# Performance work log

Hardware: AMD Instinct MI355X
Metric: run time of the kernel (lower is better)

## Reference

```python
import jax, jax.numpy as jnp
import numpy as np

B, T, C = 4, 2048, 1024
NUM_EXPERTS = 8
TOP_K = 2
D_EXPERT = 4 * C * TOP_K // NUM_EXPERTS  # 1024


def setup_inputs() -> dict:
    key = jax.random.key(0)
    k0, k1, k2, k3 = jax.random.split(key, 4)
    x = jax.random.normal(k0, (B, T, C), dtype=jnp.float32)
    # nn.Linear(n_embd, num_experts, bias=False).weight has shape [E, C]
    router_w = jax.random.normal(k1, (NUM_EXPERTS, C), dtype=jnp.float32) * 0.02
    # w1_all = stack of c_fc.weight.T  -> [E, C, D]
    w1_all = jax.random.normal(k2, (NUM_EXPERTS, C, D_EXPERT), dtype=jnp.float32) * 0.02
    # w2_all = stack of c_proj.weight.T -> [E, D, C]
    w2_all = jax.random.normal(k3, (NUM_EXPERTS, D_EXPERT, C), dtype=jnp.float32) * 0.02
    return {"x": x, "router_w": router_w, "w1_all": w1_all, "w2_all": w2_all}


def reference(x, router_w, w1_all, w2_all):
    b, t, c = x.shape
    x_flat = x.reshape(-1, c)                      # [N, C]
    router_logits = x_flat @ router_w.T            # [N, E]
    top_k_logits, top_k_idx = jax.lax.top_k(router_logits, TOP_K)  # [N, K]
    router_probs = jax.nn.softmax(top_k_logits, axis=-1)           # [N, K]

    # Same math as the original per-token weight gather, but computed as
    # dense all-expert GEMMs followed by an output gather (avoids the
    # [N, K, C, D] materialized weight copies while producing identical values).
    hidden = jnp.einsum('nc,ecd->ned', x_flat, w1_all)   # [N, E, D]
    hidden = jnp.square(jax.nn.relu(hidden))             # relu^2
    out_all = jnp.einsum('ned,edc->nec', hidden, w2_all) # [N, E, C]

    sel = jnp.take_along_axis(out_all, top_k_idx[:, :, None], axis=1)  # [N, K, C]
    out = jnp.sum(sel * router_probs[:, :, None], axis=1)             # [N, C]
    return out.reshape(b, t, c)
```

## Files before the change

### kernel.cpp

```cpp
#include <hip/hip_runtime.h>
#include <cstdint>
#include <cstddef>

typedef unsigned short ushort_t;
typedef unsigned short ushort8 __attribute__((ext_vector_type(8)));
typedef __bf16 bf16x8 __attribute__((ext_vector_type(8)));
typedef float floatx4 __attribute__((ext_vector_type(4)));

#define N_TOK 8192
#define CDIM 1024
#define NEXP 8

__device__ __forceinline__ float bf2f(ushort_t h) {
  union { unsigned int u; float f; } v; v.u = ((unsigned int)h) << 16; return v.f;
}
__device__ __forceinline__ ushort_t f2bf(float f) {
  union { float f; unsigned int u; } v; v.f = f;
  unsigned int r = v.u + 0x7fffu + ((v.u >> 16) & 1u);
  return (ushort_t)(r >> 16);
}

__device__ __forceinline__ void async_copy16(const ushort_t* g, ushort_t* l) {
  __builtin_amdgcn_global_load_lds(
      (const __attribute__((address_space(1))) unsigned int*)g,
      (__attribute__((address_space(3))) unsigned int*)l, 16, 0, 0);
}

__global__ void detect_init_kernel(const ushort_t* __restrict__ x,
                                   int* __restrict__ flag,
                                   int* __restrict__ cnt) {
  int tid = threadIdx.x;
  ushort_t u = x[tid];
  int ex = (u >> 7) & 0xFF;
  int crazy = (ex >= 0xC0 || ex <= 0x30) ? 1 : 0;
  int total = __syncthreads_count(crazy);
  if (tid == 0) flag[0] = (total >= 16) ? 1 : 0;
  if (tid < NEXP) cnt[tid] = 0;
}

__global__ void router_compute(const void* __restrict__ xv,
                               const void* __restrict__ rwv,
                               const int* __restrict__ flag,
                               int* __restrict__ tok_e,
                               float* __restrict__ prob,
                               ushort_t* __restrict__ xbf) {
  int isf32 = flag[0];
  int wid = threadIdx.x >> 6;
  int lane = threadIdx.x & 63;
  int t = blockIdx.x * 4 + wid;

  float acc[NEXP];
#pragma unroll
  for (int e = 0; e < NEXP; e++) acc[e] = 0.f;

  if (isf32) {
    const float* xr = (const float*)xv + (size_t)t * CDIM;
    const float* rw = (const float*)rwv;
#pragma unroll
    for (int half = 0; half < 2; half++) {
      int base = (lane + half * 64) * 8;
      floatx4 x0 = *(const floatx4*)(xr + base);
      floatx4 x1 = *(const floatx4*)(xr + base + 4);
      ushort8 o;
#pragma unroll
      for (int i = 0; i < 4; i++) { o[i] = f2bf(x0[i]); o[4 + i] = f2bf(x1[i]); }
      *(ushort8*)(xbf + (size_t)t * CDIM + base) = o;
#pragma unroll
      for (int e = 0; e < NEXP; e++) {
        floatx4 w0 = *(const floatx4*)(rw + e * CDIM + base);
        floatx4 w1 = *(const floatx4*)(rw + e * CDIM + base + 4);
        acc[e] += x0[0]*w0[0] + x0[1]*w0[1] + x0[2]*w0[2] + x0[3]*w0[3]
                + x1[0]*w1[0] + x1[1]*w1[1] + x1[2]*w1[2] + x1[3]*w1[3];
      }
    }
  } else {
    const ushort_t* xr = (const ushort_t*)xv + (size_t)t * CDIM;
    const ushort_t* rw = (const ushort_t*)rwv;
#pragma unroll
    for (int half = 0; half < 2; half++) {
      int base = (lane + half * 64) * 8;
      ushort8 xu = *(const ushort8*)(xr + base);
      *(ushort8*)(xbf + (size_t)t * CDIM + base) = xu;
#pragma unroll
      for (int e = 0; e < NEXP; e++) {
        ushort8 wu = *(const ushort8*)(rw + e * CDIM + base);
#pragma unroll
        for (int i = 0; i < 8; i++) acc[e] += bf2f(xu[i]) * bf2f(wu[i]);
      }
    }
  }

#pragma unroll
  for (int e = 0; e < NEXP; e++) {
#pragma unroll
    for (int off = 32; off > 0; off >>= 1) acc[e] += __shfl_xor(acc[e], off);
  }

  if (lane == 0) {
    int e0 = 0; float l0 = acc[0];
#pragma unroll
    for (int e = 1; e < NEXP; e++) if (acc[e] > l0) { l0 = acc[e]; e0 = e; }
    int e1 = (e0 == 0) ? 1 : 0; float l1 = acc[e1];
#pragma unroll
    for (int e = 0; e < NEXP; e++) {
      if (e != e0 && acc[e] > l1) { l1 = acc[e]; e1 = e; }
    }
    float p0 = 1.f / (1.f + __expf(l1 - l0));
    tok_e[t] = e0 | (e1 << 8);
    prob[t * 2] = p0;
    prob[t * 2 + 1] = 1.f - p0;
  }
}

__global__ void scatter_kernel(const int* __restrict__ tok_e,
                               int* __restrict__ cnt,
                               int* __restrict__ slots) {
  __shared__ int lcnt[NEXP];
  __shared__ int gbase[NEXP];
  int tid = threadIdx.x;
  if (tid < NEXP) lcnt[tid] = 0;
  __syncthreads();
  int t = blockIdx.x * 1024 + tid;
  int ee = tok_e[t];
  int e0 = ee & 0xFF, e1 = (ee >> 8) & 0xFF;
  int lofs0 = atomicAdd(&lcnt[e0], 1);
  int lofs1 = atomicAdd(&lcnt[e1], 1);
  __syncthreads();
  if (tid < NEXP) gbase[tid] = atomicAdd(&cnt[tid], lcnt[tid]);
  __syncthreads();
  slots[e0 * N_TOK + gbase[e0] + lofs0] = t * 2;
  slots[e1 * N_TOK + gbase[e1] + lofs1] = t * 2 + 1;
}

__global__ void transpose_kernel(const void* __restrict__ w1v,
                                 const void* __restrict__ w2v,
                                 const int* __restrict__ flag,
                                 ushort_t* __restrict__ w1T,
                                 ushort_t* __restrict__ w2T) {
  int isf32 = flag[0];
  int z = blockIdx.z;
  size_t moff = (size_t)(z & 7) << 20;
  const void* srcv = (z < 8) ? w1v : w2v;
  ushort_t* dst = ((z < 8) ? w1T : w2T) + moff;

  __shared__ __align__(16) ushort_t tile[64][72];
  int t = threadIdx.x;
  int R0 = blockIdx.y * 64, C0 = blockIdx.x * 64;
  int r = t >> 2, cb = (t & 3) * 16;
  if (isf32) {
    const float* sp = (const float*)srcv + moff + (size_t)(R0 + r) * 1024 + C0 + cb;
    ushort8 o0, o1;
#pragma unroll
    for (int q = 0; q < 2; q++) {
      floatx4 f = *(const floatx4*)(sp + q * 4);
#pragma unroll
      for (int i = 0; i < 4; i++) o0[q * 4 + i] = f2bf(f[i]);
    }
#pragma unroll
    for (int q = 0; q < 2; q++) {
      floatx4 f = *(const floatx4*)(sp + 8 + q * 4);
#pragma unroll
      for (int i = 0; i < 4; i++) o1[q * 4 + i] = f2bf(f[i]);
    }
    *(ushort8*)&tile[r][cb] = o0;
    *(ushort8*)&tile[r][cb + 8] = o1;
  } else {
    const ushort_t* sp = (const ushort_t*)srcv + moff + (size_t)(R0 + r) * 1024 + C0 + cb;
    *(ushort8*)&tile[r][cb] = *(const ushort8*)sp;
    *(ushort8*)&tile[r][cb + 8] = *(const ushort8*)(sp + 8);
  }
  __syncthreads();
  int d = t >> 2, rb = (t & 3) * 16;
  ushort8 o0, o1;
#pragma unroll
  for (int j = 0; j < 8; j++) { o0[j] = tile[rb + j][d]; o1[j] = tile[rb + 8 + j][d]; }
  ushort_t* dp = dst + (size_t)(C0 + d) * 1024 + R0 + rb;
  *(ushort8*)dp = o0;
  *(ushort8*)(dp + 8) = o1;
}

template <int MODE>
__global__ __launch_bounds__(512, 4) void moe_gemm(const ushort_t* __restrict__ A,
                                                   const ushort_t* __restrict__ BT,
                                                   ushort_t* __restrict__ Out,
                                                   const int* __restrict__ cnt,
                                                   const int* __restrict__ slots,
                                                   const float* __restrict__ prob) {
  int bid = blockIdx.x;
  int e = bid & 7;
  int nt = (bid >> 3) & 7;
  int mt = bid >> 6;
  int M = cnt[e];
  M = (M > N_TOK) ? N_TOK : M;
  int m0 = mt * 256;
  if (m0 >= M) return;
  int n0 = nt * 128;

  __shared__ __align__(16) ushort_t As[2][256 * 32];
  __shared__ __align__(16) ushort_t Bs[2][128 * 32];
  __shared__ int srow[256];

  int tid = threadIdx.x;
  if (tid < 256) {
    int gm = m0 + tid;
    int gi = (gm < M) ? gm : (M - 1);
    srow[tid] = slots[e * N_TOK + gi] & (2 * N_TOK - 1);
  }
  __syncthreads();

  int wid = tid >> 6;
  int lane = tid & 63;
  int lrow = lane >> 2;
  int gchunk = (lane & 3) ^ (lrow & 3);

  const ushort_t* aptr[2];
  const ushort_t* bptr0;
#pragma unroll
  for (int j = 0; j < 2; j++) {
    int rr = j * 128 + wid * 16 + lrow;
    int s = srow[rr];
    int aidx = (MODE == 0) ? (s >> 1) : s;
    aptr[j] = A + (size_t)aidx * CDIM + gchunk * 8;
  }
  {
    int rr = wid * 16 + lrow;
    bptr0 = BT + ((size_t)e << 20) + (size_t)(n0 + rr) * 1024 + gchunk * 8;
  }

  int wm = (wid >> 1) * 64;
  int wn = (wid & 1) * 64;
  int qd = lane >> 4;
  int ln = lane & 15;
  int l3 = ln & 3;
  int pc = (qd ^ l3) * 8;

  floatx4 zero = {0.f, 0.f, 0.f, 0.f};
  floatx4 acc[4][4];
#pragma unroll
  for (int i = 0; i < 4; i++)
#pragma unroll
    for (int j = 0; j < 4; j++) acc[i][j] = zero;

#define STAGE(buf, kofs)                                                     \
  do {                                                                       \
    async_copy16(aptr[0] + (kofs), &As[buf][wid * 512]);                     \
    async_copy16(aptr[1] + (kofs), &As[buf][4096 + wid * 512]);              \
    async_copy16(bptr0 + (kofs), &Bs[buf][wid * 512]);                       \
  } while (0)

#define COMPUTE(cb)                                                          \
  do {                                                                       \
    bf16x8 afr[4], bfr[4];                                                   \
    _Pragma("unroll")                                                        \
    for (int i = 0; i < 4; i++) {                                            \
      afr[i] = *(const bf16x8*)&As[cb][(wm + i * 16 + ln) * 32 + pc];        \
      bfr[i] = *(const bf16x8*)&Bs[cb][(wn + i * 16 + ln) * 32 + pc];        \
    }                                                                        \
    __builtin_amdgcn_s_setprio(1);                                           \
    _Pragma("unroll")                                                        \
    for (int i = 0; i < 4; i++)                                              \
      _Pragma("unroll")                                                      \
      for (int j = 0; j < 4; j++)                                            \
        acc[i][j] = __builtin_amdgcn_mfma_f32_16x16x32_bf16(afr[i], bfr[j],  \
                                                            acc[i][j], 0, 0, 0); \
    __builtin_amdgcn_s_setprio(0);                                           \
  } while (0)

  STAGE(0, 0);
  int cur = 0;
  for (int kt = 0; kt < 31; ++kt) {
    STAGE(cur ^ 1, (kt + 1) * 32);
    asm volatile("s_waitcnt vmcnt(3)" ::: "memory");
    __builtin_amdgcn_s_barrier();
    COMPUTE(cur);
    asm volatile("s_waitcnt lgkmcnt(0)" ::: "memory");
    __builtin_amdgcn_s_barrier();
    cur ^= 1;
  }
  asm volatile("s_waitcnt vmcnt(0)" ::: "memory");
  __builtin_amdgcn_s_barrier();
  COMPUTE(cur);

#undef STAGE
#undef COMPUTE

#pragma unroll
  for (int i = 0; i < 4; i++) {
#pragma unroll
    for (int r = 0; r < 4; r++) {
      int rl = wm + i * 16 + qd * 4 + r;
      int gm = m0 + rl;
      if (gm >= M) continue;
      int s = srow[rl];
      float p = (MODE == 1) ? prob[s] : 0.f;
      ushort_t* orow = Out + (size_t)s * 1024 + n0 + wn + ln;
#pragma unroll
      for (int j = 0; j < 4; j++) {
        float v = acc[i][j][r];
        if (MODE == 0) { v = fmaxf(v, 0.f); v = v * v; }
        else v *= p;
        orow[j * 16] = f2bf(v);
      }
    }
  }
}

__global__ void combine_kernel(const ushort_t* __restrict__ oslots,
                               float* __restrict__ out) {
  int idx = (blockIdx.x * 256 + threadIdx.x) * 8;
  int t = idx >> 10;
  int c = idx & 1023;
  const ushort_t* r0 = oslots + ((size_t)t * 2) * 1024 + c;
  const ushort_t* r1 = r0 + 1024;
  ushort8 a = *(const ushort8*)r0;
  ushort8 b = *(const ushort8*)r1;
  floatx4 o0, o1;
#pragma unroll
  for (int i = 0; i < 4; i++) o0[i] = bf2f(a[i]) + bf2f(b[i]);
#pragma unroll
  for (int i = 0; i < 4; i++) o1[i] = bf2f(a[4 + i]) + bf2f(b[4 + i]);
  *(floatx4*)(out + idx) = o0;
  *(floatx4*)(out + idx + 4) = o1;
}

extern "C" void kernel_launch(void* const* d_in, const int* in_sizes, int n_in,
                              void* d_out, int out_size, void* d_ws, size_t ws_size,
                              hipStream_t stream) {
  const void* x  = d_in[0];
  const void* rw = d_in[1];
  const void* w1 = d_in[2];
  const void* w2 = d_in[3];
  float* out = (float*)d_out;
  char* ws = (char*)d_ws;

  int* cnt  = (int*)(ws + 0);
  int* flag = (int*)(ws + 64);
  int* slots = (int*)(ws + 1024);
  float* prob = (float*)(ws + 263168);
  int* tok_e = (int*)(ws + 335872);
  ushort_t* xbf = (ushort_t*)(ws + 524288);
  ushort_t* w1T = (ushort_t*)(ws + 17301504);
  ushort_t* hidden = (ushort_t*)(ws + 34078720);
  ushort_t* w2T = (ushort_t*)(ws + 67633152);
  ushort_t* oslots = (ushort_t*)(ws + 524288);

  detect_init_kernel<<<1, 128, 0, stream>>>((const ushort_t*)x, flag, cnt);
  router_compute<<<N_TOK / 4, 256, 0, stream>>>(x, rw, flag, tok_e, prob, xbf);
  scatter_kernel<<<NEXP, 1024, 0, stream>>>(tok_e, cnt, slots);
  transpose_kernel<<<dim3(16, 16, 16), 256, 0, stream>>>(w1, w2, flag, w1T, w2T);
  moe_gemm<0><<<2048, 512, 0, stream>>>(xbf, w1T, hidden, cnt, slots, prob);
  moe_gemm<1><<<2048, 512, 0, stream>>>(hidden, w2T, oslots, cnt, slots, prob);
  combine_kernel<<<4096, 256, 0, stream>>>(oslots, out);
}
```

Baseline: 290.7 us.

## Triple-buffer LDS tiles, change swizzle pattern, drop setprio in MoE GEMM

Moves the MoE GEMM main loop from double to triple buffering in LDS, with a statically unrolled 3-stage rotation, so two async global-to-LDS tile loads are in flight while each tile is computed. It also changes the XOR swizzle to key on bits 1-2 of the row instead of bits 0-1, to reduce LDS bank conflicts on fragment reads, and removes the s_setprio around the MFMA block. Shared memory grows from 48KB to 72KB per block, which may reduce occupancy below the launch-bounds target of 4 blocks per CU.

```diff
diff --git a/kernel.cpp b/kernel.cpp
--- a/kernel.cpp
+++ b/kernel.cpp
@@ -196,8 +196,8 @@
   if (m0 >= M) return;
   int n0 = nt * 128;
 
-  __shared__ __align__(16) ushort_t As[2][256 * 32];
-  __shared__ __align__(16) ushort_t Bs[2][128 * 32];
+  __shared__ __align__(16) ushort_t As[3][256 * 32];
+  __shared__ __align__(16) ushort_t Bs[3][128 * 32];
   __shared__ int srow[256];
 
   int tid = threadIdx.x;
@@ -211,7 +211,7 @@
   int wid = tid >> 6;
   int lane = tid & 63;
   int lrow = lane >> 2;
-  int gchunk = (lane & 3) ^ (lrow & 3);
+  int gchunk = (lane & 3) ^ ((lrow >> 1) & 3);
 
   const ushort_t* aptr[2];
   const ushort_t* bptr0;
@@ -231,8 +231,7 @@
   int wn = (wid & 1) * 64;
   int qd = lane >> 4;
   int ln = lane & 15;
-  int l3 = ln & 3;
-  int pc = (qd ^ l3) * 8;
+  int pc = (qd ^ ((ln >> 1) & 3)) * 8;
 
   floatx4 zero = {0.f, 0.f, 0.f, 0.f};
   floatx4 acc[4][4];
@@ -241,11 +240,11 @@
 #pragma unroll
     for (int j = 0; j < 4; j++) acc[i][j] = zero;
 
-#define STAGE(buf, kofs)                                                     \
+#define STAGE(b, tile)                                                       \
   do {                                                                       \
-    async_copy16(aptr[0] + (kofs), &As[buf][wid * 512]);                     \
-    async_copy16(aptr[1] + (kofs), &As[buf][4096 + wid * 512]);              \
-    async_copy16(bptr0 + (kofs), &Bs[buf][wid * 512]);                       \
+    async_copy16(aptr[0] + (tile) * 32, &As[b][wid * 512]);                  \
+    async_copy16(aptr[1] + (tile) * 32, &As[b][4096 + wid * 512]);           \
+    async_copy16(bptr0 + (tile) * 32, &Bs[b][wid * 512]);                    \
   } while (0)
 
 #define COMPUTE(cb)                                                          \
@@ -256,33 +255,34 @@
       afr[i] = *(const bf16x8*)&As[cb][(wm + i * 16 + ln) * 32 + pc];        \
       bfr[i] = *(const bf16x8*)&Bs[cb][(wn + i * 16 + ln) * 32 + pc];        \
     }                                                                        \
-    __builtin_amdgcn_s_setprio(1);                                           \
     _Pragma("unroll")                                                        \
     for (int i = 0; i < 4; i++)                                              \
       _Pragma("unroll")                                                      \
       for (int j = 0; j < 4; j++)                                            \
         acc[i][j] = __builtin_amdgcn_mfma_f32_16x16x32_bf16(afr[i], bfr[j],  \
                                                             acc[i][j], 0, 0, 0); \
-    __builtin_amdgcn_s_setprio(0);                                           \
   } while (0)
 
+#define VMCNT(n) asm volatile("s_waitcnt vmcnt(" #n ")" ::: "memory")
+#define LGKM0()  asm volatile("s_waitcnt lgkmcnt(0)" ::: "memory")
+#define BAR()    __builtin_amdgcn_s_barrier()
+
   STAGE(0, 0);
-  int cur = 0;
-  for (int kt = 0; kt < 31; ++kt) {
-    STAGE(cur ^ 1, (kt + 1) * 32);
-    asm volatile("s_waitcnt vmcnt(3)" ::: "memory");
-    __builtin_amdgcn_s_barrier();
-    COMPUTE(cur);
-    asm volatile("s_waitcnt lgkmcnt(0)" ::: "memory");
-    __builtin_amdgcn_s_barrier();
-    cur ^= 1;
-  }
-  asm volatile("s_waitcnt vmcnt(0)" ::: "memory");
-  __builtin_amdgcn_s_barrier();
-  COMPUTE(cur);
+  STAGE(1, 1);
+  for (int it = 0; it < 10; ++it) {
+    int kt = it * 3;
+    STAGE(2, kt + 2); VMCNT(6); BAR(); COMPUTE(0); LGKM0(); BAR();
+    STAGE(0, kt + 3); VMCNT(6); BAR(); COMPUTE(1); LGKM0(); BAR();
+    STAGE(1, kt + 4); VMCNT(6); BAR(); COMPUTE(2); LGKM0(); BAR();
+  }
+  VMCNT(3); BAR(); COMPUTE(0);
+  VMCNT(0); BAR(); COMPUTE(1);
 
 #undef STAGE
 #undef COMPUTE
+#undef VMCNT
+#undef LGKM0
+#undef BAR
 
 #pragma unroll
   for (int i = 0; i < 4; i++) {
```

Result: faster. 268.8 us (-7.5%).
